# Kernel optimization log

Measured on AMD Instinct MI355X. Metric: run time of the kernel, lower is better.

The kernel has to match this reference:

```python
import jax, jax.numpy as jnp
import numpy as np

N = 2_000_000  # number of 3x3 SPD matrices (DTI-scale volume)


def _make_spd(key, n):
    # M M^T + 0.5 I is symmetric positive definite with generically distinct eigenvalues
    m = jax.random.normal(key, (n, 3, 3), dtype=jnp.float32)
    return m @ jnp.swapaxes(m, -1, -2) + 0.5 * jnp.eye(3, dtype=jnp.float32)


def setup_inputs() -> dict:
    key = jax.random.key(0)
    k1, k2 = jax.random.split(key)
    return {"D1": _make_spd(k1, N), "D2": _make_spd(k2, N)}


def _logm_spd(D):
    # Batched symmetric matrix log via eigendecomposition: V diag(log w) V^T
    w, v = jnp.linalg.eigh(D)                    # w: [N,3], v: [N,3,3]
    return (v * jnp.log(w)[..., None, :]) @ jnp.swapaxes(v, -1, -2)


def reference(D1, D2):
    # Log-Euclidean SPD distance: ||logm(D1) - logm(D2)||_F, then mean of squares
    diff = _logm_spd(D1) - _logm_spd(D2)         # [N,3,3]
    sq_dist = jnp.sum(diff * diff, axis=(-1, -2))  # [N]
    return jnp.mean(sq_dist)
```

## Files before the change

kernel.cpp:

```cpp
#include <hip/hip_runtime.h>
#include <hip/hip_bf16.h>

#define BLOCK 256
#define NWAVES 4
#define WPAIRS 64
#define WTILE_FLOATS (WPAIRS * 9)
#define WBUF_FLOATS (2 * WTILE_FLOATS)

__device__ __forceinline__ float frcp(float x) { return __builtin_amdgcn_rcpf(x); }
__device__ __forceinline__ float fsqrt(float x) { return __builtin_amdgcn_sqrtf(x); }

__device__ __forceinline__ float facos(float x) {
    float ax = fabsf(x);
    float sq = fsqrt(fmaxf(1.0f - ax, 0.0f));
    float poly = fmaf(fmaf(fmaf(-0.0187293f, ax, 0.0742610f), ax, -0.2121144f),
                      ax, 1.5707288f);
    float ac = sq * poly;
    return (x < 0.0f) ? (3.14159274f - ac) : ac;
}

__device__ __forceinline__ void logm3(const float m[6], float L[6]) {
    float a00 = m[0], a01 = m[1], a02 = m[2];
    float a11 = m[3], a12 = m[4], a22 = m[5];

    float q  = (a00 + a11 + a22) * (1.0f / 3.0f);
    float b00 = a00 - q, b11 = a11 - q, b22 = a22 - q;
    float p2 = b00*b00 + b11*b11 + b22*b22
             + 2.0f * (a01*a01 + a02*a02 + a12*a12);
    float p  = fsqrt(p2 * (1.0f / 6.0f));
    p = fmaxf(p, 1e-12f);
    float ip = frcp(p);
    float detB = b00*(b11*b22 - a12*a12)
               - a01*(a01*b22 - a12*a02)
               + a02*(a01*a12 - b11*a02);
    float ip3 = ip * ip * ip;
    float r = fminf(fmaxf(0.5f * detB * ip3, -1.0f), 1.0f);
    float phi = facos(r) * (1.0f / 3.0f);
    float sph = __sinf(phi), cph = __cosf(phi);
    float whi = q + 2.0f * p * cph;
    float wlo = q - p * (cph + 1.7320508f * sph);
    float wmid = 3.0f * q - whi - wlo;
    float w0 = fmaxf(wlo,  1e-8f);
    float w1 = fmaxf(wmid, 1e-8f);
    float w2 = fmaxf(whi,  1e-8f);

    float l0 = __logf(w0), l1 = __logf(w1), l2 = __logf(w2);
    float e = 1e-4f * w2;
    float d01 = fmaxf(w1 - w0, e);
    float d12 = fmaxf(w2 - w1, e);
    float d02 = fmaxf(w2 - w0, e);
    float rP = frcp(d01 * d12 * d02);
    float dd01 = (l1 - l0) * (d12 * d02) * rP;
    float dd12 = (l2 - l1) * (d01 * d02) * rP;
    float dd012 = (dd12 - dd01) * (d01 * d12) * rP;
    float k2 = dd012;
    float k1 = dd01 - dd012 * (w0 + w1);
    float k0 = l0 - dd01 * w0 + dd012 * (w0 * w1);

    float s00 = a00*a00 + a01*a01 + a02*a02;
    float s01 = a00*a01 + a01*a11 + a02*a12;
    float s02 = a00*a02 + a01*a12 + a02*a22;
    float s11 = a01*a01 + a11*a11 + a12*a12;
    float s12 = a01*a02 + a11*a12 + a12*a22;
    float s22 = a02*a02 + a12*a12 + a22*a22;

    L[0] = k0 + k1*a00 + k2*s00;
    L[1] =      k1*a01 + k2*s01;
    L[2] =      k1*a02 + k2*s02;
    L[3] = k0 + k1*a11 + k2*s11;
    L[4] =      k1*a12 + k2*s12;
    L[5] = k0 + k1*a22 + k2*s22;
}

__device__ __forceinline__ void load6(const float* __restrict__ a, float m[6]) {
    m[0] = a[0]; m[1] = a[1]; m[2] = a[2];
    m[3] = a[4]; m[4] = a[5]; m[5] = a[8];
}

__device__ __forceinline__ float fnorm2_diff(const float L1[6], const float L2[6]) {
    float d0 = L1[0]-L2[0], d1 = L1[1]-L2[1], d2 = L1[2]-L2[2];
    float d3 = L1[3]-L2[3], d4 = L1[4]-L2[4], d5 = L1[5]-L2[5];
    return d0*d0 + d3*d3 + d5*d5 + 2.0f * (d1*d1 + d2*d2 + d4*d4);
}

__device__ __forceinline__ void gld_lds16(const float* g, float* l) {
    __builtin_amdgcn_global_load_lds(
        (const __attribute__((address_space(1))) unsigned int*)g,
        (__attribute__((address_space(3))) unsigned int*)l, 16, 0, 0);
}
__device__ __forceinline__ void gld_lds4(const float* g, float* l) {
    __builtin_amdgcn_global_load_lds(
        (const __attribute__((address_space(1))) unsigned int*)g,
        (__attribute__((address_space(3))) unsigned int*)l, 4, 0, 0);
}

__device__ __forceinline__ void issue_wtile(float* buf,
                                            const float* __restrict__ D1,
                                            const float* __restrict__ D2,
                                            long t, int lane) {
    const float* s1 = D1 + t * WTILE_FLOATS;
    const float* s2 = D2 + t * WTILE_FLOATS;
    gld_lds16(s1 +       lane * 4, buf);
    gld_lds16(s1 + 256 + lane * 4, buf + 256);
    gld_lds4 (s1 + 512 + lane,     buf + 512);
    gld_lds16(s2 +       lane * 4, buf + 576);
    gld_lds16(s2 + 256 + lane * 4, buf + 832);
    gld_lds4 (s2 + 512 + lane,     buf + 1088);
}

__global__ void __launch_bounds__(BLOCK)
le_partial(const float* __restrict__ D1, const float* __restrict__ D2,
           float* __restrict__ partial, int n) {
    __shared__ __align__(16) float lds[NWAVES * 2 * WBUF_FLOATS];
    const int tid  = threadIdx.x;
    const int wave = tid >> 6, lane = tid & 63;
    float* wlds = lds + wave * (2 * WBUF_FLOATS);

    const long ntw = n / WPAIRS;
    const long W   = (long)gridDim.x * NWAVES;
    long t = (long)blockIdx.x * NWAVES + wave;
    float acc = 0.0f;

    if (t < ntw) {
        issue_wtile(wlds, D1, D2, t, lane);
        int cur = 0;
        while (true) {
            long tn = t + W;
            bool hn = (tn < ntw);
            if (hn) issue_wtile(wlds + (cur ^ 1) * WBUF_FLOATS, D1, D2, tn, lane);

            if (hn) asm volatile("s_waitcnt vmcnt(6)" ::: "memory");
            else    asm volatile("s_waitcnt vmcnt(0)" ::: "memory");
            __builtin_amdgcn_sched_barrier(0);

            const float* b = wlds + cur * WBUF_FLOATS;
            float m1[6], m2[6], L1[6], L2[6];
            load6(b + lane * 9, m1);
            load6(b + WTILE_FLOATS + lane * 9, m2);
            logm3(m1, L1);
            logm3(m2, L2);
            acc += fnorm2_diff(L1, L2);

            if (!hn) break;
            cur ^= 1;
            t = tn;
        }
    }

    {
        long base = ntw * WPAIRS;
        if (blockIdx.x == 0 && (long)tid < n - base) {
            long ti = base + tid;
            float m1[6], m2[6], L1[6], L2[6];
            load6(D1 + ti * 9, m1);
            load6(D2 + ti * 9, m2);
            logm3(m1, L1);
            logm3(m2, L2);
            acc += fnorm2_diff(L1, L2);
        }
    }

    #pragma unroll
    for (int off = 32; off > 0; off >>= 1)
        acc += __shfl_down(acc, off, 64);
    __shared__ float wsum[NWAVES];
    if (lane == 0) wsum[wave] = acc;
    __syncthreads();
    if (tid == 0) {
        float s = 0.0f;
        #pragma unroll
        for (int j = 0; j < NWAVES; ++j) s += wsum[j];
        partial[blockIdx.x] = s;
    }
}

__global__ void __launch_bounds__(BLOCK)
le_final(const float* __restrict__ partial, int nparts,
         float* __restrict__ out, double invN) {
    double s = 0.0;
    for (int i = threadIdx.x; i < nparts; i += BLOCK)
        s += (double)partial[i];
    #pragma unroll
    for (int off = 32; off > 0; off >>= 1)
        s += __shfl_down(s, off, 64);
    __shared__ double ws[BLOCK / 64];
    if ((threadIdx.x & 63) == 0) ws[threadIdx.x >> 6] = s;
    __syncthreads();
    if (threadIdx.x == 0) {
        double tt = 0.0;
        #pragma unroll
        for (int i = 0; i < BLOCK / 64; ++i) tt += ws[i];
        out[0] = (float)(tt * invN);
    }
}

extern "C" void kernel_launch(void* const* d_in, const int* in_sizes, int n_in,
                              void* d_out, int out_size, void* d_ws, size_t ws_size,
                              hipStream_t stream) {
    const float* D1 = (const float*)d_in[0];
    const float* D2 = (const float*)d_in[1];
    float* out = (float*)d_out;
    float* partial = (float*)d_ws;

    int n = in_sizes[0] / 9;
    long ntw = n / WPAIRS;

    int grid = 1024;
    long maxg = (ntw + NWAVES - 1) / NWAVES;
    if (maxg > 0 && grid > maxg) grid = (int)maxg;
    int maxblocks = (int)(ws_size / sizeof(float));
    if (maxblocks > 0 && grid > maxblocks) grid = maxblocks;
    if (grid < 1) grid = 1;

    le_partial<<<grid, BLOCK, 0, stream>>>(D1, D2, partial, n);
    le_final<<<1, BLOCK, 0, stream>>>(partial, grid, out, 1.0 / (double)n);
}
```

Measured before the change: 33.54 us.

## Deepen per-wave LDS prefetch ring to three stages and stagger wave starts

Replaces the double-buffered global-to-LDS prefetch with a three-deep ring per wave, issuing the next tile right after reading the current one so more memory requests stay in flight. Blocks shrink to three waves and the grid to 768, keeping the total wave count, and waves start with staggered s_sleep delays to spread DRAM request bursts. The eigenvalue setup uses a single rsq instead of sqrt plus rcp. The trade-off is more LDS per block and more complex drain logic.

```diff
diff --git a/kernel.cpp b/kernel.cpp
--- a/kernel.cpp
+++ b/kernel.cpp
@@ -1,14 +1,23 @@
 #include <hip/hip_runtime.h>
 #include <hip/hip_bf16.h>
 
-#define BLOCK 256
-#define NWAVES 4
+#define BLOCK 192
+#define NWAVES 3
+#define DEPTH 3
 #define WPAIRS 64
 #define WTILE_FLOATS (WPAIRS * 9)
 #define WBUF_FLOATS (2 * WTILE_FLOATS)
+#define FBLOCK 256
 
 __device__ __forceinline__ float frcp(float x) { return __builtin_amdgcn_rcpf(x); }
 __device__ __forceinline__ float fsqrt(float x) { return __builtin_amdgcn_sqrtf(x); }
+__device__ __forceinline__ float frsq(float x) { return __builtin_amdgcn_rsqf(x); }
+
+#define SB() __builtin_amdgcn_sched_barrier(0)
+__device__ __forceinline__ void waitv12() { asm volatile("s_waitcnt vmcnt(12)" ::: "memory"); SB(); }
+__device__ __forceinline__ void waitv6()  { asm volatile("s_waitcnt vmcnt(6)"  ::: "memory"); SB(); }
+__device__ __forceinline__ void waitv0()  { asm volatile("s_waitcnt vmcnt(0)"  ::: "memory"); SB(); }
+__device__ __forceinline__ void waitl0()  { asm volatile("s_waitcnt lgkmcnt(0)" ::: "memory"); SB(); }
 
 __device__ __forceinline__ float facos(float x) {
     float ax = fabsf(x);
@@ -27,9 +36,9 @@
     float b00 = a00 - q, b11 = a11 - q, b22 = a22 - q;
     float p2 = b00*b00 + b11*b11 + b22*b22
              + 2.0f * (a01*a01 + a02*a02 + a12*a12);
-    float p  = fsqrt(p2 * (1.0f / 6.0f));
-    p = fmaxf(p, 1e-12f);
-    float ip = frcp(p);
+    float u  = fmaxf(p2 * (1.0f / 6.0f), 1e-24f);
+    float ip = frsq(u);
+    float p  = u * ip;
     float detB = b00*(b11*b22 - a12*a12)
                - a01*(a01*b22 - a12*a02)
                + a02*(a01*a12 - b11*a02);
@@ -83,6 +92,13 @@
     return d0*d0 + d3*d3 + d5*d5 + 2.0f * (d1*d1 + d2*d2 + d4*d4);
 }
 
+__device__ __forceinline__ float pairdist(const float m1[6], const float m2[6]) {
+    float L1[6], L2[6];
+    logm3(m1, L1);
+    logm3(m2, L2);
+    return fnorm2_diff(L1, L2);
+}
+
 __device__ __forceinline__ void gld_lds16(const float* g, float* l) {
     __builtin_amdgcn_global_load_lds(
         (const __attribute__((address_space(1))) unsigned int*)g,
@@ -108,55 +124,94 @@
     gld_lds4 (s2 + 512 + lane,     buf + 1088);
 }
 
+__device__ __forceinline__ void readpair(const float* b, int lane,
+                                         float m1[6], float m2[6]) {
+    load6(b + lane * 9, m1);
+    load6(b + WTILE_FLOATS + lane * 9, m2);
+}
+
 __global__ void __launch_bounds__(BLOCK)
 le_partial(const float* __restrict__ D1, const float* __restrict__ D2,
            float* __restrict__ partial, int n) {
-    __shared__ __align__(16) float lds[NWAVES * 2 * WBUF_FLOATS];
+    __shared__ __align__(16) float lds[NWAVES * DEPTH * WBUF_FLOATS];
     const int tid  = threadIdx.x;
     const int wave = tid >> 6, lane = tid & 63;
-    float* wlds = lds + wave * (2 * WBUF_FLOATS);
+    float* wlds = lds + wave * (DEPTH * WBUF_FLOATS);
+
+    unsigned ph = ((unsigned)blockIdx.x * 5u + (unsigned)wave * 3u) & 7u;
+    switch (ph) {
+        case 1: __builtin_amdgcn_s_sleep(3);  break;
+        case 2: __builtin_amdgcn_s_sleep(6);  break;
+        case 3: __builtin_amdgcn_s_sleep(9);  break;
+        case 4: __builtin_amdgcn_s_sleep(12); break;
+        case 5: __builtin_amdgcn_s_sleep(15); break;
+        case 6: __builtin_amdgcn_s_sleep(18); break;
+        case 7: __builtin_amdgcn_s_sleep(21); break;
+        default: break;
+    }
 
     const long ntw = n / WPAIRS;
     const long W   = (long)gridDim.x * NWAVES;
-    long t = (long)blockIdx.x * NWAVES + wave;
+    const long base = (long)blockIdx.x * NWAVES + wave;
     float acc = 0.0f;
 
-    if (t < ntw) {
-        issue_wtile(wlds, D1, D2, t, lane);
+    if (base < ntw) {
+        bool h1 = base + W < ntw, h2 = base + 2 * W < ntw;
+        issue_wtile(wlds, D1, D2, base, lane);
+        if (h1) issue_wtile(wlds + WBUF_FLOATS,     D1, D2, base + W,     lane);
+        if (h2) issue_wtile(wlds + 2 * WBUF_FLOATS, D1, D2, base + 2 * W, lane);
+
+        long t   = base;
+        long tis = base + 3 * W;
         int cur = 0;
-        while (true) {
-            long tn = t + W;
-            bool hn = (tn < ntw);
-            if (hn) issue_wtile(wlds + (cur ^ 1) * WBUF_FLOATS, D1, D2, tn, lane);
-
-            if (hn) asm volatile("s_waitcnt vmcnt(6)" ::: "memory");
-            else    asm volatile("s_waitcnt vmcnt(0)" ::: "memory");
-            __builtin_amdgcn_sched_barrier(0);
-
-            const float* b = wlds + cur * WBUF_FLOATS;
-            float m1[6], m2[6], L1[6], L2[6];
-            load6(b + lane * 9, m1);
-            load6(b + WTILE_FLOATS + lane * 9, m2);
-            logm3(m1, L1);
-            logm3(m2, L2);
-            acc += fnorm2_diff(L1, L2);
-
-            if (!hn) break;
-            cur ^= 1;
-            t = tn;
+
+        while (tis < ntw) {
+            waitv12();
+            float m1[6], m2[6];
+            readpair(wlds + cur * WBUF_FLOATS, lane, m1, m2);
+            waitl0();
+            issue_wtile(wlds + cur * WBUF_FLOATS, D1, D2, tis, lane);
+            SB();
+            acc += pairdist(m1, m2);
+            tis += W; t += W;
+            cur = (cur == DEPTH - 1) ? 0 : cur + 1;
         }
+
+        {
+            bool e1 = (t + W) < ntw, e2 = (t + 2 * W) < ntw;
+            if (e2) waitv12(); else if (e1) waitv6(); else waitv0();
+            {
+                float m1[6], m2[6];
+                readpair(wlds + cur * WBUF_FLOATS, lane, m1, m2);
+                acc += pairdist(m1, m2);
+            }
+            if (e1) {
+                cur = (cur == DEPTH - 1) ? 0 : cur + 1;
+                if (e2) waitv6(); else waitv0();
+                {
+                    float m1[6], m2[6];
+                    readpair(wlds + cur * WBUF_FLOATS, lane, m1, m2);
+                    acc += pairdist(m1, m2);
+                }
+                if (e2) {
+                    cur = (cur == DEPTH - 1) ? 0 : cur + 1;
+                    waitv0();
+                    float m1[6], m2[6];
+                    readpair(wlds + cur * WBUF_FLOATS, lane, m1, m2);
+                    acc += pairdist(m1, m2);
+                }
+            }
+        }
     }
 
     {
-        long base = ntw * WPAIRS;
-        if (blockIdx.x == 0 && (long)tid < n - base) {
-            long ti = base + tid;
-            float m1[6], m2[6], L1[6], L2[6];
+        long tb = ntw * WPAIRS;
+        if (blockIdx.x == 0 && (long)tid < n - tb) {
+            long ti = tb + tid;
+            float m1[6], m2[6];
             load6(D1 + ti * 9, m1);
             load6(D2 + ti * 9, m2);
-            logm3(m1, L1);
-            logm3(m2, L2);
-            acc += fnorm2_diff(L1, L2);
+            acc += pairdist(m1, m2);
         }
     }
 
@@ -174,22 +229,22 @@
     }
 }
 
-__global__ void __launch_bounds__(BLOCK)
+__global__ void __launch_bounds__(FBLOCK)
 le_final(const float* __restrict__ partial, int nparts,
          float* __restrict__ out, double invN) {
     double s = 0.0;
-    for (int i = threadIdx.x; i < nparts; i += BLOCK)
+    for (int i = threadIdx.x; i < nparts; i += FBLOCK)
         s += (double)partial[i];
     #pragma unroll
     for (int off = 32; off > 0; off >>= 1)
         s += __shfl_down(s, off, 64);
-    __shared__ double ws[BLOCK / 64];
+    __shared__ double ws[FBLOCK / 64];
     if ((threadIdx.x & 63) == 0) ws[threadIdx.x >> 6] = s;
     __syncthreads();
     if (threadIdx.x == 0) {
         double tt = 0.0;
         #pragma unroll
-        for (int i = 0; i < BLOCK / 64; ++i) tt += ws[i];
+        for (int i = 0; i < FBLOCK / 64; ++i) tt += ws[i];
         out[0] = (float)(tt * invN);
     }
 }
@@ -205,7 +260,7 @@
     int n = in_sizes[0] / 9;
     long ntw = n / WPAIRS;
 
-    int grid = 1024;
+    int grid = 768;
     long maxg = (ntw + NWAVES - 1) / NWAVES;
     if (maxg > 0 && grid > maxg) grid = (int)maxg;
     int maxblocks = (int)(ws_size / sizeof(float));
@@ -213,5 +268,5 @@
     if (grid < 1) grid = 1;
 
     le_partial<<<grid, BLOCK, 0, stream>>>(D1, D2, partial, n);
-    le_final<<<1, BLOCK, 0, stream>>>(partial, grid, out, 1.0 / (double)n);
-}
+    le_final<<<1, FBLOCK, 0, stream>>>(partial, grid, out, 1.0 / (double)n);
+}
```

Measured after the change: 38.47 us. 1.15x slower.
